# Kernel optimization log

Measured on AMD Instinct MI355X. Metric: run time of the kernel, lower is better.

Reference implementation:

```python
import jax, jax.numpy as jnp
import numpy as np

E, B, N, F, F1D, H, L, H2, PE_DIM = 4, 16384, 1024, 64, 64, 256, 2, 256, 63
TOPK_MEM = 16      # self.top_K: memory retrieval top-k
W0_SIREN = 30.0    # SIREN omega_0 for 'sine' nonlinearity
NUM_FREQ = 10      # PosEncoding num_frequencies
LINE_DIM = 64      # feat_shapes[0]


def _ln(h, g, b):
    m = jnp.mean(h, axis=-1, keepdims=True)
    v = jnp.mean((h - m) ** 2, axis=-1, keepdims=True)
    return (h - m) / jnp.sqrt(v + 1e-5) * g + b


def _pos_enc(coords):
    # NeRF positional encoding: [coords, sin/cos interleaved per coord per freq]
    freqs = 2.0 ** jnp.arange(NUM_FREQ, dtype=coords.dtype)
    scaled = coords[..., None] * freqs * jnp.pi            # (B, 3, NF)
    sc = jnp.stack([jnp.sin(scaled), jnp.cos(scaled)], axis=-1)  # (B, 3, NF, 2)
    return jnp.concatenate([coords, sc.reshape(coords.shape[0], -1)], axis=-1)  # (B, 63)


def _forward(x, lines, mem_k, mem_v, enc_w0, enc_b0, enc_wh, enc_bh, enc_wo, enc_bo,
             ln_g, ln_b, wq, wk, wv, ad_w0, ad_b0, ad_w1, ad_b1, ad_ln_g, ad_ln_b,
             mg_w0, mg_b0, mg_w1, mg_b1, fw0, fb0, fw1, fb1, fw2, fb2, fw3, fb3, route_k):
    coords = x[:, :3]
    # --- 1D line feature interpolation (param_feats) ---
    p = x[:, 3] * (LINE_DIM - 1)
    pf = jnp.floor(p)
    w = p - pf
    il = pf.astype(jnp.int32)
    ih = jnp.clip(pf + 1.0, 0.0, LINE_DIM - 1).astype(jnp.int32)
    f1d = lines[0][:, il] + w * (lines[0][:, ih] - lines[0][:, il])  # (F1D, B)
    param_feats = f1d.T                                              # (B, F1D)

    pe_x = _pos_enc(coords)                                          # (B, 63)
    scale = float(F) ** 0.5

    def expert(ew0, eb0, ewh, ebh, ewo, ebo, wq_e, wk_e, wv_e, mk, mv,
               aw0, ab0, aw1, ab1, ag, ab):
        # SIREN encoder MLP
        h = jnp.sin(W0_SIREN * (pe_x @ ew0 + eb0))
        for l in range(L):
            h = jnp.sin(W0_SIREN * (h @ ewh[l] + ebh[l]))
        mlp_feats = h @ ewo + ebo                          # (B, F)
        q = _ln(mlp_feats, ln_g, ln_b) @ wq_e              # (B, F)
        kp = mk @ wk_e                                     # (N, F) precomputed keys
        vp = mv @ wv_e                                     # (N, F) precomputed values
        scores = q @ kp.T                                  # (B, N)
        _, idx = jax.lax.top_k(scores, TOPK_MEM)           # (B, K)
        k_top = kp[idx]                                    # (B, K, F)
        v_top = vp[idx]                                    # (B, K, F)
        pfe = jnp.broadcast_to(param_feats[:, None, :], (param_feats.shape[0], TOPK_MEM, F1D))
        a = jnp.concatenate([v_top, pfe], axis=-1)         # (B, K, F+F1D)
        a = jax.nn.relu(a @ aw0 + ab0) @ aw1 + ab1
        adapted = v_top + _ln(a, ag, ab)
        attn = jax.nn.softmax(jnp.einsum('bf,bkf->bk', q, k_top) / scale, axis=-1)
        return jnp.einsum('bk,bkf->bf', attn, adapted) + mlp_feats

    # compute every expert densely (vectorized), then gather routed top-k outputs
    all_out = jax.vmap(expert)(enc_w0, enc_b0, enc_wh, enc_bh, enc_wo, enc_bo,
                               wq, wk, wv, mem_k, mem_v,
                               ad_w0, ad_b0, ad_w1, ad_b1, ad_ln_g, ad_ln_b)  # (E, B, F)

    raw_q = jax.nn.relu(coords @ mg_w0 + mg_b0) @ mg_w1 + mg_b1   # manager_net (B, E)
    probs = jnp.clip(jax.nn.softmax(raw_q, axis=-1), 1e-8, None)
    vals, tidx = jax.lax.top_k(probs, route_k)                    # (B, k)
    vals = vals / jnp.sum(vals, axis=-1, keepdims=True)
    gathered = jnp.take_along_axis(jnp.swapaxes(all_out, 0, 1), tidx[..., None], axis=1)  # (B, k, F)
    spatial = jnp.sum(vals[..., None] * gathered, axis=1)         # (B, F)

    h = jax.nn.relu(spatial @ fw0 + fb0)
    h = jax.nn.relu(h @ fw1 + fb1)
    h = jax.nn.relu(h @ fw2 + fb2)
    refined = jax.nn.sigmoid(h @ fw3 + fb3)
    return refined, raw_q


def setup_inputs() -> dict:
    ks = jax.random.split(jax.random.key(0), 24)
    f32 = jnp.float32
    rn = lambda i, shp, s: jax.random.normal(ks[i], shp, f32) * s
    xav = lambda fi, fo: (2.0 / (fi + fo)) ** 0.5
    return {
        'x': jax.random.uniform(ks[0], (B, 4), f32),
        'lines': jax.random.uniform(ks[1], (1, F1D, LINE_DIM), f32, 0.7, 0.8),
        'mem_k': rn(2, (E, N, F), 1.0),
        'mem_v': rn(3, (E, N, F), 1e-3),
        'enc_w0': rn(4, (E, PE_DIM, H), xav(PE_DIM, H)),
        'enc_b0': jnp.zeros((E, H), f32),
        'enc_wh': rn(5, (E, L, H, H), xav(H, H)),
        'enc_bh': jnp.zeros((E, L, H), f32),
        'enc_wo': rn(6, (E, H, F), xav(H, F)),
        'enc_bo': jnp.zeros((E, F), f32),
        'ln_g': jnp.ones((F,), f32),
        'ln_b': jnp.zeros((F,), f32),
        'wq': rn(7, (E, F, F), xav(F, F)),
        'wk': rn(8, (E, F, F), xav(F, F)),
        'wv': rn(9, (E, F, F), xav(F, F)),
        'ad_w0': rn(10, (E, F + F1D, 64), xav(F + F1D, 64)),
        'ad_b0': rn(11, (E, 64), 1e-3),
        'ad_w1': rn(12, (E, 64, F), xav(64, F)),
        'ad_b1': rn(13, (E, F), 1e-3),
        'ad_ln_g': jnp.ones((E, F), f32),
        'ad_ln_b': jnp.zeros((E, F), f32),
        'mg_w0': rn(14, (3, 64), 0.5),
        'mg_b0': jnp.zeros((64,), f32),
        'mg_w1': rn(15, (64, E), 0.5),
        'mg_b1': jnp.zeros((E,), f32),
        'fw0': rn(16, (F, H2), xav(F, H2)),
        'fb0': rn(17, (H2,), 1e-3),
        'fw1': rn(18, (H2, H2), xav(H2, H2)),
        'fb1': rn(19, (H2,), 1e-3),
        'fw2': rn(20, (H2, H2), xav(H2, H2)),
        'fb2': rn(21, (H2,), 1e-3),
        'fw3': rn(22, (H2, 1), xav(H2, 1)),
        'fb3': rn(23, (1,), 1e-3),
        'route_k': 2,
    }


def reference(x, lines, mem_k, mem_v, enc_w0, enc_b0, enc_wh, enc_bh, enc_wo, enc_bo,
              ln_g, ln_b, wq, wk, wv, ad_w0, ad_b0, ad_w1, ad_b1, ad_ln_g, ad_ln_b,
              mg_w0, mg_b0, mg_w1, mg_b1, fw0, fb0, fw1, fb1, fw2, fb2, fw3, fb3, route_k):
    return _forward(x, lines, mem_k, mem_v, enc_w0, enc_b0, enc_wh, enc_bh, enc_wo, enc_bo,
                    ln_g, ln_b, wq, wk, wv, ad_w0, ad_b0, ad_w1, ad_b1, ad_ln_g, ad_ln_b,
                    mg_w0, mg_b0, mg_w1, mg_b1, fw0, fb0, fw1, fb1, fw2, fb2, fw3, fb3, route_k)
```

## Files before the change

kernel.cpp:

```cpp
#include <hip/hip_runtime.h>
#include <math.h>

#define EE 4
#define BB 16384
#define NN 1024
#define FF 64
#define HH 256
#define PED 63
#define TOPK 16
#define LINE 64
#define TS 32
#define NBX (BB/TS)

#define OFF_KP   0u
#define OFF_VP   262144u
#define OFF_VPA  524288u
#define OFF_PE   786432u
#define OFF_PF   1818624u
#define OFF_EO   2867200u
#define OFF_RW   4964352u
#define OFF_CNT  4997120u
#define OFF_LIST 4997128u
#define OFF_QV   5062664u
#define OFF_SM   7159816u
#define OFF_WP   OFF_EO

__device__ __forceinline__ float wred_sum(float v) {
#pragma unroll
    for (int off = 32; off > 0; off >>= 1) v += __shfl_xor(v, off, 64);
    return v;
}
__device__ __forceinline__ void wred_sum2(float& a, float& b) {
#pragma unroll
    for (int off = 32; off > 0; off >>= 1) {
        a += __shfl_xor(a, off, 64);
        b += __shfl_xor(b, off, 64);
    }
}

__global__ __launch_bounds__(256) void k_prep(
    const float* __restrict__ wv, const float* __restrict__ aw0,
    float* __restrict__ wp)
{
    int e = blockIdx.x;
    __shared__ float sa[FF*FF];
    for (int i = threadIdx.x; i < FF*FF; i += 256)
        sa[i] = aw0[(size_t)e*128*FF + i];
    __syncthreads();
    int f = threadIdx.x & 63, dg = threadIdx.x >> 6;
    for (int d = dg; d < FF; d += 4) {
        const float* wr = wv + (size_t)e*FF*FF + d*FF;
        float a = 0.f;
        for (int c = 0; c < FF; ++c) a = fmaf(wr[c], sa[c*FF+f], a);
        wp[(size_t)e*FF*FF + d*FF + f] = a;
    }
}

__global__ __launch_bounds__(256) void k_proj(
    const float* __restrict__ mem_k, const float* __restrict__ mem_v,
    const float* __restrict__ wk, const float* __restrict__ wv,
    const float* __restrict__ wp,
    float* __restrict__ kp, float* __restrict__ vp, float* __restrict__ vpa)
{
    int e = blockIdx.x >> 6;
    int nbase = (blockIdx.x & 63) * 16;
    __shared__ float swk[FF*FF], swv[FF*FF], swp[FF*FF];
    for (int i = threadIdx.x; i < FF*FF; i += 256) {
        swk[i] = wk[(size_t)e*FF*FF + i];
        swv[i] = wv[(size_t)e*FF*FF + i];
        swp[i] = wp[(size_t)e*FF*FF + i];
    }
    __syncthreads();
    int r4 = threadIdx.x >> 6;
    int f  = threadIdx.x & 63;
#pragma unroll 1
    for (int it = 0; it < 4; ++it) {
        int n = nbase + it*4 + r4;
        const float* mk = mem_k + ((size_t)e*NN + n)*FF;
        const float* mv = mem_v + ((size_t)e*NN + n)*FF;
        float ak = 0.f, av = 0.f, aa = 0.f;
#pragma unroll 1
        for (int c4 = 0; c4 < 16; ++c4) {
            float4 k4 = *(const float4*)&mk[4*c4];
            float4 v4 = *(const float4*)&mv[4*c4];
#pragma unroll
            for (int kk = 0; kk < 4; ++kk) {
                float mkc = (kk==0)?k4.x:((kk==1)?k4.y:((kk==2)?k4.z:k4.w));
                float mvc = (kk==0)?v4.x:((kk==1)?v4.y:((kk==2)?v4.z:v4.w));
                int c = 4*c4 + kk;
                ak = fmaf(mkc, swk[c*FF+f], ak);
                av = fmaf(mvc, swv[c*FF+f], av);
                aa = fmaf(mvc, swp[c*FF+f], aa);
            }
        }
        kp [((size_t)e*NN+n)*FF + f] = ak;
        vp [((size_t)e*NN+n)*FF + f] = av;
        vpa[((size_t)e*NN+n)*FF + f] = aa;
    }
}

__global__ __launch_bounds__(256) void k_route(
    const float* __restrict__ x, const float* __restrict__ lines,
    const float* __restrict__ mg_w0, const float* __restrict__ mg_b0,
    const float* __restrict__ mg_w1, const float* __restrict__ mg_b1,
    float* __restrict__ pe_x, float* __restrict__ pfm,
    float* __restrict__ rawq, float* __restrict__ rw,
    int* __restrict__ counts, int* __restrict__ lists)
{
    __shared__ float slines[LINE*LINE];
    for (int i = threadIdx.x; i < LINE*LINE; i += 256) slines[i] = lines[i];
    __syncthreads();
    int b = blockIdx.x*256 + threadIdx.x;
    float4 xx = ((const float4*)x)[b];
    float c0 = xx.x, c1 = xx.y, c2 = xx.z, c3 = xx.w;

    float p = c3 * (float)(LINE-1);
    float pfl = floorf(p);
    float w = p - pfl;
    int il = (int)pfl;
    int ih = (int)fminf(fmaxf(pfl + 1.f, 0.f), (float)(LINE-1));
    for (int c = 0; c < FF; ++c) {
        float lo = slines[c*LINE+il], hi = slines[c*LINE+ih];
        pfm[(size_t)b*FF + c] = lo + w*(hi-lo);
    }
    float* pe = pe_x + (size_t)b*PED;
    pe[0]=c0; pe[1]=c1; pe[2]=c2;
    const float PI = 3.14159265358979323846f;
    float coords[3] = {c0,c1,c2};
#pragma unroll
    for (int cc = 0; cc < 3; ++cc) {
        float fr = PI;
        for (int k = 0; k < 10; ++k) {
            float s = coords[cc]*fr;
            pe[3 + cc*20 + k*2 + 0] = sinf(s);
            pe[3 + cc*20 + k*2 + 1] = cosf(s);
            fr *= 2.f;
        }
    }
    float acc[4] = {mg_b1[0], mg_b1[1], mg_b1[2], mg_b1[3]};
    for (int j = 0; j < 64; ++j) {
        float h = fmaf(c0, mg_w0[j], fmaf(c1, mg_w0[64+j], fmaf(c2, mg_w0[128+j], mg_b0[j])));
        h = fmaxf(h, 0.f);
#pragma unroll
        for (int e4 = 0; e4 < 4; ++e4) acc[e4] = fmaf(h, mg_w1[j*4+e4], acc[e4]);
    }
#pragma unroll
    for (int e4 = 0; e4 < 4; ++e4) rawq[(size_t)b*4 + e4] = acc[e4];
    float m = fmaxf(fmaxf(acc[0],acc[1]), fmaxf(acc[2],acc[3]));
    float ex[4], den = 0.f;
#pragma unroll
    for (int e4 = 0; e4 < 4; ++e4) { ex[e4] = expf(acc[e4]-m); den += ex[e4]; }
    float pr[4];
#pragma unroll
    for (int e4 = 0; e4 < 4; ++e4) pr[e4] = fmaxf(ex[e4]/den, 1e-8f);
    int i0 = 0;
#pragma unroll
    for (int e4 = 1; e4 < 4; ++e4) if (pr[e4] > pr[i0]) i0 = e4;
    int i1 = -1;
#pragma unroll
    for (int e4 = 0; e4 < 4; ++e4) {
        if (e4 == i0) continue;
        if (i1 < 0 || pr[e4] > pr[i1]) i1 = e4;
    }
    float vs = pr[i0] + pr[i1];
    rw[b*2+0] = pr[i0]/vs;
    rw[b*2+1] = pr[i1]/vs;
    int p0 = atomicAdd(&counts[i0], 1);
    lists[i0*BB + p0] = b*2 + 0;
    int p1 = atomicAdd(&counts[i1], 1);
    lists[i1*BB + p1] = b*2 + 1;
}

__global__ __launch_bounds__(512, 6) void k_mlp(
    const float* __restrict__ pe_x,
    const float* __restrict__ enc_w0, const float* __restrict__ enc_b0,
    const float* __restrict__ enc_wh, const float* __restrict__ enc_bh,
    const float* __restrict__ enc_wo, const float* __restrict__ enc_bo,
    const float* __restrict__ ln_g, const float* __restrict__ ln_b,
    const float* __restrict__ wq,
    const int* __restrict__ counts, const int* __restrict__ lists,
    float* __restrict__ qv, float* __restrict__ smlpw)
{
    const int e = blockIdx.y;
    const int base = blockIdx.x * TS;
    const int cnt = counts[e];
    if (base >= cnt) return;

    __shared__ float sh[TS*HH];
    __shared__ float swt[4096];
    __shared__ int   slist[TS];

    const int tid = threadIdx.x;
    const int lane = tid & 63;
    const int wv = tid >> 6;
    const int r0 = wv*4;

    if (tid < TS) {
        int idx = base + tid;
        if (idx >= cnt) idx = cnt - 1;
        slist[tid] = lists[e*BB + idx];
    }
    __syncthreads();
    for (int i = tid; i < TS*64; i += 512) {
        int s = i >> 6, j = i & 63;
        int bq = slist[s] >> 1;
        sh[s*HH + j] = (j < PED) ? pe_x[(size_t)bq*PED + j] : 0.f;
    }

    float acc[4][4];

    {
        const float* W = enc_w0 + (size_t)e*PED*HH;
#pragma unroll
        for (int s = 0; s < 4; ++s)
#pragma unroll
            for (int j = 0; j < 4; ++j) acc[s][j] = 0.f;
#pragma unroll 1
        for (int t = 0; t < 4; ++t) {
            int rbase = t*16;
            int rows = (PED - rbase < 16) ? (PED - rbase) : 16;
            int total = rows*HH;
            __syncthreads();
            for (int i = tid*4; i < total; i += 2048)
                *(float4*)&swt[i] = *(const float4*)&W[rbase*HH + i];
            __syncthreads();
#pragma unroll 1
            for (int k = 0; k < rows; ++k) {
                float4 w4 = *(const float4*)&swt[k*HH + 4*lane];
#pragma unroll
                for (int s = 0; s < 4; ++s) {
                    float hv = sh[(r0+s)*HH + rbase + k];
                    acc[s][0] = fmaf(hv, w4.x, acc[s][0]);
                    acc[s][1] = fmaf(hv, w4.y, acc[s][1]);
                    acc[s][2] = fmaf(hv, w4.z, acc[s][2]);
                    acc[s][3] = fmaf(hv, w4.w, acc[s][3]);
                }
            }
        }
        __syncthreads();
        float4 b4 = *(const float4*)&enc_b0[e*HH + 4*lane];
#pragma unroll
        for (int s = 0; s < 4; ++s) {
            float4 o;
            o.x = sinf(30.0f*(acc[s][0] + b4.x));
            o.y = sinf(30.0f*(acc[s][1] + b4.y));
            o.z = sinf(30.0f*(acc[s][2] + b4.z));
            o.w = sinf(30.0f*(acc[s][3] + b4.w));
            *(float4*)&sh[(r0+s)*HH + 4*lane] = o;
        }
    }

#pragma unroll 1
    for (int layer = 0; layer < 2; ++layer) {
        const float* W = enc_wh + ((size_t)(e*2+layer))*HH*HH;
#pragma unroll
        for (int s = 0; s < 4; ++s)
#pragma unroll
            for (int j = 0; j < 4; ++j) acc[s][j] = 0.f;
#pragma unroll 1
        for (int t = 0; t < 16; ++t) {
            __syncthreads();
            for (int i = tid*4; i < 4096; i += 2048)
                *(float4*)&swt[i] = *(const float4*)&W[t*16*HH + i];
            __syncthreads();
#pragma unroll 1
            for (int k4 = 0; k4 < 4; ++k4) {
                float4 h4[4];
#pragma unroll
                for (int s = 0; s < 4; ++s)
                    h4[s] = *(const float4*)&sh[(r0+s)*HH + t*16 + 4*k4];
#pragma unroll
                for (int kk = 0; kk < 4; ++kk) {
                    float4 w4 = *(const float4*)&swt[(4*k4+kk)*HH + 4*lane];
#pragma unroll
                    for (int s = 0; s < 4; ++s) {
                        float hv = (kk==0)?h4[s].x:((kk==1)?h4[s].y:((kk==2)?h4[s].z:h4[s].w));
                        acc[s][0] = fmaf(hv, w4.x, acc[s][0]);
                        acc[s][1] = fmaf(hv, w4.y, acc[s][1]);
                        acc[s][2] = fmaf(hv, w4.z, acc[s][2]);
                        acc[s][3] = fmaf(hv, w4.w, acc[s][3]);
                    }
                }
            }
        }
        __syncthreads();
        float4 b4 = *(const float4*)&enc_bh[(e*2+layer)*HH + 4*lane];
#pragma unroll
        for (int s = 0; s < 4; ++s) {
            float4 o;
            o.x = sinf(30.0f*(acc[s][0] + b4.x));
            o.y = sinf(30.0f*(acc[s][1] + b4.y));
            o.z = sinf(30.0f*(acc[s][2] + b4.z));
            o.w = sinf(30.0f*(acc[s][3] + b4.w));
            *(float4*)&sh[(r0+s)*HH + 4*lane] = o;
        }
    }

    float smlp_r[4];
    {
        const float* W = enc_wo + (size_t)e*HH*FF;
        float a2o[4] = {0.f,0.f,0.f,0.f};
#pragma unroll 1
        for (int t = 0; t < 4; ++t) {
            __syncthreads();
            for (int i = tid*4; i < 4096; i += 2048)
                *(float4*)&swt[i] = *(const float4*)&W[t*64*FF + i];
            __syncthreads();
#pragma unroll 1
            for (int k4 = 0; k4 < 16; ++k4) {
                float4 h4[4];
#pragma unroll
                for (int s = 0; s < 4; ++s)
                    h4[s] = *(const float4*)&sh[(r0+s)*HH + t*64 + 4*k4];
#pragma unroll
                for (int kk = 0; kk < 4; ++kk) {
                    float w = swt[(4*k4+kk)*FF + lane];
#pragma unroll
                    for (int s = 0; s < 4; ++s) {
                        float hv = (kk==0)?h4[s].x:((kk==1)?h4[s].y:((kk==2)?h4[s].z:h4[s].w));
                        a2o[s] = fmaf(hv, w, a2o[s]);
                    }
                }
            }
        }
        float bv = enc_bo[e*FF + lane];
#pragma unroll
        for (int s = 0; s < 4; ++s) smlp_r[s] = a2o[s] + bv;
    }

    {
        const float* Wq = wq + (size_t)e*FF*FF;
        __syncthreads();
        for (int i = tid*4; i < 4096; i += 2048)
            *(float4*)&swt[i] = *(const float4*)&Wq[i];
        __syncthreads();
        float g = ln_g[lane], bb2 = ln_b[lane];
#pragma unroll 1
        for (int s = 0; s < 4; ++s) {
            float hv = smlp_r[s];
            float sm = hv, s2 = hv*hv;
            wred_sum2(sm, s2);
            float mean = sm * (1.f/64.f);
            float var = s2 * (1.f/64.f) - mean*mean;
            float lnv = (hv - mean) * rsqrtf(var + 1e-5f) * g + bb2;
            sh[(r0+s)*HH + lane] = lnv;
            float qa = 0.f;
#pragma unroll 1
            for (int c4 = 0; c4 < 16; ++c4) {
                float4 l4 = *(const float4*)&sh[(r0+s)*HH + 4*c4];
                qa = fmaf(l4.x, swt[(4*c4+0)*FF + lane], qa);
                qa = fmaf(l4.y, swt[(4*c4+1)*FF + lane], qa);
                qa = fmaf(l4.z, swt[(4*c4+2)*FF + lane], qa);
                qa = fmaf(l4.w, swt[(4*c4+3)*FF + lane], qa);
            }
            if (base + r0 + s < cnt) {
                size_t entry = (size_t)slist[r0+s];
                qv[entry*FF + lane] = qa;
                smlpw[entry*FF + lane] = smlp_r[s];
            }
        }
    }
}

__global__ __launch_bounds__(512, 4) void k_attn(
    const float* __restrict__ pfm,
    const float* __restrict__ kp, const float* __restrict__ vp,
    const float* __restrict__ vpa,
    const float* __restrict__ qv, const float* __restrict__ smlpw,
    const float* __restrict__ aw0, const float* __restrict__ ab0,
    const float* __restrict__ aw1, const float* __restrict__ ab1,
    const float* __restrict__ adg, const float* __restrict__ adb,
    const int* __restrict__ counts, const int* __restrict__ lists,
    float* __restrict__ eo)
{
    const int e = blockIdx.y;
    const int base = blockIdx.x * TS;
    const int cnt = counts[e];
    if (base >= cnt) return;

    __shared__ float swt[8192];
    __shared__ float sq[TS*FF];
    __shared__ float pl[8*1024];
    __shared__ float wr_l[8*TOPK];
    __shared__ int   slist[TS];

    const int tid = threadIdx.x;
    const int lane = tid & 63;
    const int wv = tid >> 6;
    const int r0 = wv*4;

    if (tid < TS) {
        int idx = base + tid;
        if (idx >= cnt) idx = cnt - 1;
        slist[tid] = lists[e*BB + idx];
    }
    __syncthreads();
    for (int i = tid; i < TS*64; i += 512) {
        int s = i >> 6, c = i & 63;
        sq[i] = qv[(size_t)slist[s]*FF + c];
    }

    float sc[4][16];
    {
        const float* kpe = kp + (size_t)e*NN*FF;
        const int str = tid >> 3;
        const int stc = (tid & 7) * 8;
#pragma unroll 1
        for (int c = 0; c < 16; ++c) {
            __syncthreads();
            {
                const float* src = kpe + (size_t)(c*64 + str)*FF + stc;
                float* dst = &swt[str*68 + stc];
                *(float4*)(dst+0) = *(const float4*)(src+0);
                *(float4*)(dst+4) = *(const float4*)(src+4);
            }
            __syncthreads();
            float a0 = 0.f, a1 = 0.f, a2s = 0.f, a3 = 0.f;
#pragma unroll
            for (int f4 = 0; f4 < 16; ++f4) {
                float4 k4 = *(const float4*)&swt[lane*68 + 4*f4];
                float4 q0 = *(const float4*)&sq[(r0+0)*FF + 4*f4];
                float4 q1 = *(const float4*)&sq[(r0+1)*FF + 4*f4];
                float4 q2 = *(const float4*)&sq[(r0+2)*FF + 4*f4];
                float4 q3 = *(const float4*)&sq[(r0+3)*FF + 4*f4];
                a0 = fmaf(k4.x,q0.x,fmaf(k4.y,q0.y,fmaf(k4.z,q0.z,fmaf(k4.w,q0.w,a0))));
                a1 = fmaf(k4.x,q1.x,fmaf(k4.y,q1.y,fmaf(k4.z,q1.z,fmaf(k4.w,q1.w,a1))));
                a2s= fmaf(k4.x,q2.x,fmaf(k4.y,q2.y,fmaf(k4.z,q2.z,fmaf(k4.w,q2.w,a2s))));
                a3 = fmaf(k4.x,q3.x,fmaf(k4.y,q3.y,fmaf(k4.z,q3.z,fmaf(k4.w,q3.w,a3))));
            }
            sc[0][c]=a0; sc[1][c]=a1; sc[2][c]=a2s; sc[3][c]=a3;
        }
    }

    __syncthreads();
    {
        const float* a0bG = aw0 + ((size_t)e*128 + 64)*FF;
        const float* w1G  = aw1 + (size_t)e*FF*FF;
        for (int i = tid*4; i < 4096; i += 2048) {
            *(float4*)&swt[i]        = *(const float4*)&a0bG[i];
            *(float4*)&swt[4096 + i] = *(const float4*)&w1G[i];
        }
    }
    __syncthreads();

    const float* vpe  = vp  + (size_t)e*NN*FF;
    const float* vpae = vpa + (size_t)e*NN*FF;
    const float agv = adg[e*FF + lane], abv = adb[e*FF + lane];
    const float ab0v = ab0[e*FF + lane];
    const float ab1v = ab1[e*FF + lane];
    float* plw = &pl[wv*1024];

#pragma unroll
    for (int u = 0; u < 4; ++u) {
        int s = r0 + u;
        int entry = slist[s];
        int bq = entry >> 1;

        float pp = ab0v;
        {
            const float* pfr = pfm + (size_t)bq*FF;
#pragma unroll 1
            for (int c4 = 0; c4 < 16; ++c4) {
                float4 p4 = *(const float4*)&pfr[4*c4];
                pp = fmaf(p4.x, swt[(4*c4+0)*FF + lane], pp);
                pp = fmaf(p4.y, swt[(4*c4+1)*FF + lane], pp);
                pp = fmaf(p4.z, swt[(4*c4+2)*FF + lane], pp);
                pp = fmaf(p4.w, swt[(4*c4+3)*FF + lane], pp);
            }
        }

        int rns[16];
        unsigned taken = 0u;
        bool need = true;
        float bv = -1e30f; int bn = 0x7fffffff;
        float v0max = 0.f, wsum = 0.f;
#pragma unroll
        for (int r = 0; r < TOPK; ++r) {
            if (need) {
                bv = -1e30f; bn = 0x7fffffff;
#pragma unroll
                for (int c = 0; c < 16; ++c) {
                    float v = sc[u][c];
                    int n = c*64 + lane;
                    bool ok = !((taken >> c) & 1u);
                    bool better = ok && (v > bv || (v == bv && n < bn));
                    bv = better ? v : bv;
                    bn = better ? n : bn;
                }
                need = false;
            }
            float rv = bv; int rn = bn;
#pragma unroll
            for (int off = 32; off > 0; off >>= 1) {
                float ov = __shfl_xor(rv, off, 64);
                int on = __shfl_xor(rn, off, 64);
                bool better = (ov > rv) || (ov == rv && on < rn);
                rv = better ? ov : rv;
                rn = better ? on : rn;
            }
            if (r == 0) v0max = rv;
            float wr = expf((rv - v0max) * 0.125f);
            wsum += wr;
            if (lane == 0) wr_l[wv*TOPK + r] = wr;
            if ((rn & 63) == lane) { taken |= 1u << (rn >> 6); need = true; }
            rns[r] = rn;
        }

        float pav[16];
#pragma unroll
        for (int r = 0; r < TOPK; ++r)
            pav[r] = vpae[(size_t)rns[r]*FF + lane];
#pragma unroll
        for (int q = 0; q < 4; ++q) {
            int slot = q ^ (lane & 3);
            float4 o;
            o.x = fmaxf(pav[4*q+0] + pp, 0.f);
            o.y = fmaxf(pav[4*q+1] + pp, 0.f);
            o.z = fmaxf(pav[4*q+2] + pp, 0.f);
            o.w = fmaxf(pav[4*q+3] + pp, 0.f);
            *(float4*)&plw[lane*16 + slot*4] = o;
        }
        float a2[16];
#pragma unroll
        for (int r = 0; r < 16; ++r) a2[r] = ab1v;
#pragma unroll 1
        for (int j4 = 0; j4 < 16; ++j4) {
            const float* plj = &plw[j4*64];
#pragma unroll
            for (int jj = 0; jj < 4; ++jj) {
                float w = swt[4096 + (4*j4+jj)*FF + lane];
#pragma unroll
                for (int lq = 0; lq < 4; ++lq) {
                    float4 d = *(const float4*)&plj[jj*16 + ((lq ^ jj) * 4)];
                    a2[4*lq+0] = fmaf(d.x, w, a2[4*lq+0]);
                    a2[4*lq+1] = fmaf(d.y, w, a2[4*lq+1]);
                    a2[4*lq+2] = fmaf(d.z, w, a2[4*lq+2]);
                    a2[4*lq+3] = fmaf(d.w, w, a2[4*lq+3]);
                }
            }
        }
        float vvt[16];
#pragma unroll
        for (int r = 0; r < TOPK; ++r)
            vvt[r] = vpe[(size_t)rns[r]*FF + lane];
        float outacc = 0.f;
#pragma unroll
        for (int r = 0; r < TOPK; ++r) {
            float av = a2[r];
            float sm = av, s2 = av*av;
            wred_sum2(sm, s2);
            float mean = sm * (1.f/64.f);
            float var = s2 * (1.f/64.f) - mean*mean;
            float lnv = (av - mean) * rsqrtf(var + 1e-5f) * agv + abv;
            outacc = fmaf(wr_l[wv*TOPK + r], vvt[r] + lnv, outacc);
        }
        float res = outacc / wsum + smlpw[(size_t)entry*FF + lane];
        if (base + s < cnt) eo[(size_t)entry*FF + lane] = res;
    }
}

__global__ __launch_bounds__(512, 6) void k_final(
    const float* __restrict__ eo, const float* __restrict__ rw,
    const float* __restrict__ fw0, const float* __restrict__ fb0,
    const float* __restrict__ fw1, const float* __restrict__ fb1,
    const float* __restrict__ fw2, const float* __restrict__ fb2,
    const float* __restrict__ fw3, const float* __restrict__ fb3,
    float* __restrict__ refined)
{
    __shared__ float sh[TS*HH];
    __shared__ float swt[4096];
    const int tid = threadIdx.x, lane = tid & 63, wv = tid >> 6;
    const int sbase = blockIdx.x * TS;
    const int r0 = wv*4;
    for (int i = tid; i < TS*64; i += 512) {
        int s = i >> 6, c = i & 63;
        int b = sbase + s;
        sh[s*HH + c] = rw[b*2]*eo[(size_t)(b*2)*FF + c]
                     + rw[b*2+1]*eo[(size_t)(b*2+1)*FF + c];
    }
    float acc[4][4];
    {
#pragma unroll
        for (int s = 0; s < 4; ++s)
#pragma unroll
            for (int j = 0; j < 4; ++j) acc[s][j] = 0.f;
#pragma unroll 1
        for (int t = 0; t < 4; ++t) {
            __syncthreads();
            for (int i = tid*4; i < 4096; i += 2048)
                *(float4*)&swt[i] = *(const float4*)&fw0[t*16*HH + i];
            __syncthreads();
#pragma unroll 1
            for (int k = 0; k < 16; ++k) {
                float4 w4 = *(const float4*)&swt[k*HH + 4*lane];
#pragma unroll
                for (int s = 0; s < 4; ++s) {
                    float hv = sh[(r0+s)*HH + t*16 + k];
                    acc[s][0] = fmaf(hv, w4.x, acc[s][0]);
                    acc[s][1] = fmaf(hv, w4.y, acc[s][1]);
                    acc[s][2] = fmaf(hv, w4.z, acc[s][2]);
                    acc[s][3] = fmaf(hv, w4.w, acc[s][3]);
                }
            }
        }
        __syncthreads();
        float4 b4 = *(const float4*)&fb0[4*lane];
#pragma unroll
        for (int s = 0; s < 4; ++s) {
            float4 o;
            o.x = fmaxf(acc[s][0] + b4.x, 0.f);
            o.y = fmaxf(acc[s][1] + b4.y, 0.f);
            o.z = fmaxf(acc[s][2] + b4.z, 0.f);
            o.w = fmaxf(acc[s][3] + b4.w, 0.f);
            *(float4*)&sh[(r0+s)*HH + 4*lane] = o;
        }
    }
#pragma unroll 1
    for (int layer = 0; layer < 2; ++layer) {
        const float* W  = layer ? fw2 : fw1;
        const float* bi = layer ? fb2 : fb1;
#pragma unroll
        for (int s = 0; s < 4; ++s)
#pragma unroll
            for (int j = 0; j < 4; ++j) acc[s][j] = 0.f;
#pragma unroll 1
        for (int t = 0; t < 16; ++t) {
            __syncthreads();
            for (int i = tid*4; i < 4096; i += 2048)
                *(float4*)&swt[i] = *(const float4*)&W[t*16*HH + i];
            __syncthreads();
#pragma unroll 1
            for (int k4 = 0; k4 < 4; ++k4) {
                float4 h4[4];
#pragma unroll
                for (int s = 0; s < 4; ++s)
                    h4[s] = *(const float4*)&sh[(r0+s)*HH + t*16 + 4*k4];
#pragma unroll
                for (int kk = 0; kk < 4; ++kk) {
                    float4 w4 = *(const float4*)&swt[(4*k4+kk)*HH + 4*lane];
#pragma unroll
                    for (int s = 0; s < 4; ++s) {
                        float hv = (kk==0)?h4[s].x:((kk==1)?h4[s].y:((kk==2)?h4[s].z:h4[s].w));
                        acc[s][0] = fmaf(hv, w4.x, acc[s][0]);
                        acc[s][1] = fmaf(hv, w4.y, acc[s][1]);
                        acc[s][2] = fmaf(hv, w4.z, acc[s][2]);
                        acc[s][3] = fmaf(hv, w4.w, acc[s][3]);
                    }
                }
            }
        }
        __syncthreads();
        float4 b4 = *(const float4*)&bi[4*lane];
#pragma unroll
        for (int s = 0; s < 4; ++s) {
            float4 o;
            o.x = fmaxf(acc[s][0] + b4.x, 0.f);
            o.y = fmaxf(acc[s][1] + b4.y, 0.f);
            o.z = fmaxf(acc[s][2] + b4.z, 0.f);
            o.w = fmaxf(acc[s][3] + b4.w, 0.f);
            *(float4*)&sh[(r0+s)*HH + 4*lane] = o;
        }
    }
    {
        float4 w4 = *(const float4*)&fw3[4*lane];
#pragma unroll 1
        for (int s = 0; s < 4; ++s) {
            float4 h4 = *(const float4*)&sh[(r0+s)*HH + 4*lane];
            float part = h4.x*w4.x + h4.y*w4.y + h4.z*w4.z + h4.w*w4.w;
            float tot = wred_sum(part) + fb3[0];
            float r = 1.f/(1.f + expf(-tot));
            if (lane == 0) refined[sbase + r0 + s] = r;
        }
    }
}

extern "C" void kernel_launch(void* const* d_in, const int* in_sizes, int n_in,
                              void* d_out, int out_size, void* d_ws, size_t ws_size,
                              hipStream_t stream)
{
    const float* x      = (const float*)d_in[0];
    const float* lines  = (const float*)d_in[1];
    const float* mem_k  = (const float*)d_in[2];
    const float* mem_v  = (const float*)d_in[3];
    const float* enc_w0 = (const float*)d_in[4];
    const float* enc_b0 = (const float*)d_in[5];
    const float* enc_wh = (const float*)d_in[6];
    const float* enc_bh = (const float*)d_in[7];
    const float* enc_wo = (const float*)d_in[8];
    const float* enc_bo = (const float*)d_in[9];
    const float* ln_g   = (const float*)d_in[10];
    const float* ln_b   = (const float*)d_in[11];
    const float* wq     = (const float*)d_in[12];
    const float* wk     = (const float*)d_in[13];
    const float* wv_    = (const float*)d_in[14];
    const float* ad_w0  = (const float*)d_in[15];
    const float* ad_b0  = (const float*)d_in[16];
    const float* ad_w1  = (const float*)d_in[17];
    const float* ad_b1  = (const float*)d_in[18];
    const float* ad_g   = (const float*)d_in[19];
    const float* ad_b   = (const float*)d_in[20];
    const float* mg_w0  = (const float*)d_in[21];
    const float* mg_b0  = (const float*)d_in[22];
    const float* mg_w1  = (const float*)d_in[23];
    const float* mg_b1  = (const float*)d_in[24];
    const float* fw0    = (const float*)d_in[25];
    const float* fb0    = (const float*)d_in[26];
    const float* fw1    = (const float*)d_in[27];
    const float* fb1    = (const float*)d_in[28];
    const float* fw2    = (const float*)d_in[29];
    const float* fb2    = (const float*)d_in[30];
    const float* fw3    = (const float*)d_in[31];
    const float* fb3    = (const float*)d_in[32];

    float* out_ref = (float*)d_out;
    float* out_rq  = (float*)d_out + BB;

    float* ws  = (float*)d_ws;
    float* kp  = ws + OFF_KP;
    float* vp  = ws + OFF_VP;
    float* vpa = ws + OFF_VPA;
    float* pe  = ws + OFF_PE;
    float* pfm = ws + OFF_PF;
    float* eo  = ws + OFF_EO;
    float* rw  = ws + OFF_RW;
    float* qvw = ws + OFF_QV;
    float* smw = ws + OFF_SM;
    float* wpw = ws + OFF_WP;
    int*  cnts = (int*)(ws + OFF_CNT);
    int*  lst  = (int*)(ws + OFF_LIST);

    hipMemsetAsync(cnts, 0, EE*sizeof(int), stream);
    k_prep<<<dim3(EE), dim3(256), 0, stream>>>(wv_, ad_w0, wpw);
    k_proj<<<dim3(EE*64), dim3(256), 0, stream>>>(mem_k, mem_v, wk, wv_, wpw, kp, vp, vpa);
    k_route<<<dim3(BB/256), dim3(256), 0, stream>>>(x, lines, mg_w0, mg_b0, mg_w1, mg_b1,
                                                    pe, pfm, out_rq, rw, cnts, lst);
    k_mlp<<<dim3(NBX, EE), dim3(512), 0, stream>>>(pe,
        enc_w0, enc_b0, enc_wh, enc_bh, enc_wo, enc_bo, ln_g, ln_b, wq,
        cnts, lst, qvw, smw);
    k_attn<<<dim3(NBX, EE), dim3(512), 0, stream>>>(pfm, kp, vp, vpa, qvw, smw,
        ad_w0, ad_b0, ad_w1, ad_b1, ad_g, ad_b, cnts, lst, eo);
    k_final<<<dim3(BB/TS), dim3(512), 0, stream>>>(eo, rw, fw0, fb0, fw1, fb1,
                                                   fw2, fb2, fw3, fb3, out_ref);
}
```

Before: 1.225 ms.

## Enlarge attention tile to 64 rows with 1024-thread blocks and overlapped loads

The attention kernel now processes 64 routed samples per block with 1024 threads, so each key tile staged in shared memory serves twice as many queries. Shared memory is reorganised into a union buffer plus dedicated adapter-weight arrays that are loaded up front instead of after the score loop, which drops one barrier. Top-k weights stay in registers via readfirstlane rather than shared memory, and the value and adapter-value gathers are merged and issued earlier. Larger blocks may lower occupancy and raise register pressure.

Result: slower. 1.469 ms (+19.9%).

```diff
diff --git a/kernel.cpp b/kernel.cpp
--- a/kernel.cpp
+++ b/kernel.cpp
@@ -11,6 +11,8 @@
 #define LINE 64
 #define TS 32
 #define NBX (BB/TS)
+#define TSA 64
+#define NBA 256
 
 #define OFF_KP   0u
 #define OFF_VP   262144u
@@ -362,7 +364,7 @@
     }
 }
 
-__global__ __launch_bounds__(512, 4) void k_attn(
+__global__ __launch_bounds__(1024, 4) void k_attn(
     const float* __restrict__ pfm,
     const float* __restrict__ kp, const float* __restrict__ vp,
     const float* __restrict__ vpa,
@@ -374,71 +376,63 @@
     float* __restrict__ eo)
 {
     const int e = blockIdx.y;
-    const int base = blockIdx.x * TS;
+    const int base = blockIdx.x * TSA;
     const int cnt = counts[e];
     if (base >= cnt) return;
 
-    __shared__ float swt[8192];
-    __shared__ float sq[TS*FF];
-    __shared__ float pl[8*1024];
-    __shared__ float wr_l[8*TOPK];
-    __shared__ int   slist[TS];
+    __shared__ float su[16384];
+    __shared__ float sa0[4096];
+    __shared__ float sw1[4096];
+    __shared__ int   slist[TSA];
+
+    float* sq  = su;
+    float* skp = su + 4096;
 
     const int tid = threadIdx.x;
     const int lane = tid & 63;
     const int wv = tid >> 6;
     const int r0 = wv*4;
 
-    if (tid < TS) {
+    if (tid < TSA) {
         int idx = base + tid;
         if (idx >= cnt) idx = cnt - 1;
         slist[tid] = lists[e*BB + idx];
     }
     __syncthreads();
-    for (int i = tid; i < TS*64; i += 512) {
-        int s = i >> 6, c = i & 63;
-        sq[i] = qv[(size_t)slist[s]*FF + c];
+    {
+        int s4 = tid >> 4, c4 = (tid & 15)*4;
+        *(float4*)&sq[s4*64 + c4] = *(const float4*)&qv[(size_t)slist[s4]*FF + c4];
+        const float* a0bG = aw0 + ((size_t)e*128 + 64)*FF;
+        const float* w1G  = aw1 + (size_t)e*FF*FF;
+        *(float4*)&sa0[tid*4] = *(const float4*)&a0bG[tid*4];
+        *(float4*)&sw1[tid*4] = *(const float4*)&w1G[tid*4];
     }
 
     float sc[4][16];
     {
         const float* kpe = kp + (size_t)e*NN*FF;
-        const int str = tid >> 3;
-        const int stc = (tid & 7) * 8;
+        const int str = tid >> 4;
+        const int stc = (tid & 15) * 4;
 #pragma unroll 1
         for (int c = 0; c < 16; ++c) {
             __syncthreads();
-            {
-                const float* src = kpe + (size_t)(c*64 + str)*FF + stc;
-                float* dst = &swt[str*68 + stc];
-                *(float4*)(dst+0) = *(const float4*)(src+0);
-                *(float4*)(dst+4) = *(const float4*)(src+4);
-            }
+            *(float4*)&skp[str*68 + stc] =
+                *(const float4*)&kpe[(size_t)(c*64 + str)*FF + stc];
             __syncthreads();
             float a0 = 0.f, a1 = 0.f, a2s = 0.f, a3 = 0.f;
 #pragma unroll
             for (int f4 = 0; f4 < 16; ++f4) {
-                float4 k4 = *(const float4*)&swt[lane*68 + 4*f4];
-                float4 q0 = *(const float4*)&sq[(r0+0)*FF + 4*f4];
-                float4 q1 = *(const float4*)&sq[(r0+1)*FF + 4*f4];
-                float4 q2 = *(const float4*)&sq[(r0+2)*FF + 4*f4];
-                float4 q3 = *(const float4*)&sq[(r0+3)*FF + 4*f4];
+                float4 k4 = *(const float4*)&skp[lane*68 + 4*f4];
+                float4 q0 = *(const float4*)&sq[(r0+0)*64 + 4*f4];
+                float4 q1 = *(const float4*)&sq[(r0+1)*64 + 4*f4];
+                float4 q2 = *(const float4*)&sq[(r0+2)*64 + 4*f4];
+                float4 q3 = *(const float4*)&sq[(r0+3)*64 + 4*f4];
                 a0 = fmaf(k4.x,q0.x,fmaf(k4.y,q0.y,fmaf(k4.z,q0.z,fmaf(k4.w,q0.w,a0))));
                 a1 = fmaf(k4.x,q1.x,fmaf(k4.y,q1.y,fmaf(k4.z,q1.z,fmaf(k4.w,q1.w,a1))));
                 a2s= fmaf(k4.x,q2.x,fmaf(k4.y,q2.y,fmaf(k4.z,q2.z,fmaf(k4.w,q2.w,a2s))));
                 a3 = fmaf(k4.x,q3.x,fmaf(k4.y,q3.y,fmaf(k4.z,q3.z,fmaf(k4.w,q3.w,a3))));
             }
             sc[0][c]=a0; sc[1][c]=a1; sc[2][c]=a2s; sc[3][c]=a3;
-        }
-    }
-
-    __syncthreads();
-    {
-        const float* a0bG = aw0 + ((size_t)e*128 + 64)*FF;
-        const float* w1G  = aw1 + (size_t)e*FF*FF;
-        for (int i = tid*4; i < 4096; i += 2048) {
-            *(float4*)&swt[i]        = *(const float4*)&a0bG[i];
-            *(float4*)&swt[4096 + i] = *(const float4*)&w1G[i];
         }
     }
     __syncthreads();
@@ -448,7 +442,7 @@
     const float agv = adg[e*FF + lane], abv = adb[e*FF + lane];
     const float ab0v = ab0[e*FF + lane];
     const float ab1v = ab1[e*FF + lane];
-    float* plw = &pl[wv*1024];
+    float* plw = &su[wv*1024];
 
 #pragma unroll
     for (int u = 0; u < 4; ++u) {
@@ -462,14 +456,15 @@
 #pragma unroll 1
             for (int c4 = 0; c4 < 16; ++c4) {
                 float4 p4 = *(const float4*)&pfr[4*c4];
-                pp = fmaf(p4.x, swt[(4*c4+0)*FF + lane], pp);
-                pp = fmaf(p4.y, swt[(4*c4+1)*FF + lane], pp);
-                pp = fmaf(p4.z, swt[(4*c4+2)*FF + lane], pp);
-                pp = fmaf(p4.w, swt[(4*c4+3)*FF + lane], pp);
+                pp = fmaf(p4.x, sa0[(4*c4+0)*FF + lane], pp);
+                pp = fmaf(p4.y, sa0[(4*c4+1)*FF + lane], pp);
+                pp = fmaf(p4.z, sa0[(4*c4+2)*FF + lane], pp);
+                pp = fmaf(p4.w, sa0[(4*c4+3)*FF + lane], pp);
             }
         }
 
         int rns[16];
+        float wrs[16];
         unsigned taken = 0u;
         bool need = true;
         float bv = -1e30f; int bn = 0x7fffffff;
@@ -498,27 +493,39 @@
                 rv = better ? ov : rv;
                 rn = better ? on : rn;
             }
+            int rn_u = __builtin_amdgcn_readfirstlane(rn);
             if (r == 0) v0max = rv;
             float wr = expf((rv - v0max) * 0.125f);
             wsum += wr;
-            if (lane == 0) wr_l[wv*TOPK + r] = wr;
-            if ((rn & 63) == lane) { taken |= 1u << (rn >> 6); need = true; }
-            rns[r] = rn;
-        }
-
-        float pav[16];
-#pragma unroll
-        for (int r = 0; r < TOPK; ++r)
-            pav[r] = vpae[(size_t)rns[r]*FF + lane];
-#pragma unroll
-        for (int q = 0; q < 4; ++q) {
-            int slot = q ^ (lane & 3);
-            float4 o;
-            o.x = fmaxf(pav[4*q+0] + pp, 0.f);
-            o.y = fmaxf(pav[4*q+1] + pp, 0.f);
-            o.z = fmaxf(pav[4*q+2] + pp, 0.f);
-            o.w = fmaxf(pav[4*q+3] + pp, 0.f);
-            *(float4*)&plw[lane*16 + slot*4] = o;
+            if ((rn_u & 63) == lane) { taken |= 1u << (rn_u >> 6); need = true; }
+            rns[r] = rn_u;
+            wrs[r] = wr;
+        }
+
+        float oaccv = 0.f;
+#pragma unroll
+        for (int g2 = 0; g2 < 2; ++g2) {
+            float pav[8], vv[8];
+#pragma unroll
+            for (int r8 = 0; r8 < 8; ++r8) {
+                int r = g2*8 + r8;
+                pav[r8] = vpae[(size_t)rns[r]*FF + lane];
+                vv[r8]  = vpe [(size_t)rns[r]*FF + lane];
+            }
+#pragma unroll
+            for (int r8 = 0; r8 < 8; ++r8)
+                oaccv = fmaf(wrs[g2*8 + r8], vv[r8], oaccv);
+#pragma unroll
+            for (int q = 0; q < 2; ++q) {
+                int qq = g2*2 + q;
+                int slot = qq ^ (lane & 3);
+                float4 o;
+                o.x = fmaxf(pav[4*q+0] + pp, 0.f);
+                o.y = fmaxf(pav[4*q+1] + pp, 0.f);
+                o.z = fmaxf(pav[4*q+2] + pp, 0.f);
+                o.w = fmaxf(pav[4*q+3] + pp, 0.f);
+                *(float4*)&plw[lane*16 + slot*4] = o;
+            }
         }
         float a2[16];
 #pragma unroll
@@ -528,7 +535,7 @@
             const float* plj = &plw[j4*64];
 #pragma unroll
             for (int jj = 0; jj < 4; ++jj) {
-                float w = swt[4096 + (4*j4+jj)*FF + lane];
+                float w = sw1[(4*j4+jj)*FF + lane];
 #pragma unroll
                 for (int lq = 0; lq < 4; ++lq) {
                     float4 d = *(const float4*)&plj[jj*16 + ((lq ^ jj) * 4)];
@@ -539,11 +546,7 @@
                 }
             }
         }
-        float vvt[16];
-#pragma unroll
-        for (int r = 0; r < TOPK; ++r)
-            vvt[r] = vpe[(size_t)rns[r]*FF + lane];
-        float outacc = 0.f;
+        float oln = 0.f;
 #pragma unroll
         for (int r = 0; r < TOPK; ++r) {
             float av = a2[r];
@@ -552,9 +555,9 @@
             float mean = sm * (1.f/64.f);
             float var = s2 * (1.f/64.f) - mean*mean;
             float lnv = (av - mean) * rsqrtf(var + 1e-5f) * agv + abv;
-            outacc = fmaf(wr_l[wv*TOPK + r], vvt[r] + lnv, outacc);
-        }
-        float res = outacc / wsum + smlpw[(size_t)entry*FF + lane];
+            oln = fmaf(wrs[r], lnv, oln);
+        }
+        float res = (oaccv + oln) / wsum + smlpw[(size_t)entry*FF + lane];
         if (base + s < cnt) eo[(size_t)entry*FF + lane] = res;
     }
 }
@@ -737,7 +740,7 @@
     k_mlp<<<dim3(NBX, EE), dim3(512), 0, stream>>>(pe,
         enc_w0, enc_b0, enc_wh, enc_bh, enc_wo, enc_bo, ln_g, ln_b, wq,
         cnts, lst, qvw, smw);
-    k_attn<<<dim3(NBX, EE), dim3(512), 0, stream>>>(pfm, kp, vp, vpa, qvw, smw,
+    k_attn<<<dim3(NBA, EE), dim3(1024), 0, stream>>>(pfm, kp, vp, vpa, qvw, smw,
         ad_w0, ad_b0, ad_w1, ad_b1, ad_g, ad_b, cnts, lst, eo);
     k_final<<<dim3(BB/TS), dim3(512), 0, stream>>>(eo, rw, fw0, fb0, fw1, fb1,
                                                    fw2, fb2, fw3, fb3, out_ref);
```
